# Kernel tuning notes

Measured on AMD Instinct MI355X. Metric: run time of the kernel, lower is better.

The kernel has to match this reference:

```python
import jax, jax.numpy as jnp
import numpy as np

EMB = 512       # emb_dim
H = 8           # n_heads
HD = EMB // H   # head_dim = 64
FREQ = 64       # freq_features
PERIOD = 0.1
N = 2048


def setup_inputs() -> dict:
    key = jax.random.key(0)
    ks = jax.random.split(key, 6)
    x = jax.random.normal(ks[0], (1, N, EMB), dtype=jnp.float32)
    v = jax.random.normal(ks[1], (1, N, 3), dtype=jnp.float32)
    vec_map = v / jnp.linalg.norm(v, axis=-1, keepdims=True)  # unit direction vectors
    s_in = 1.0 / np.sqrt(EMB)
    W_qkv = jax.random.normal(ks[2], (EMB, 3 * EMB), dtype=jnp.float32) * s_in
    b_qkv = jnp.zeros((3 * EMB,), dtype=jnp.float32)
    W_bias = jax.random.normal(ks[3], (FREQ, H), dtype=jnp.float32) * (1.0 / np.sqrt(FREQ))
    b_bias = jnp.zeros((H,), dtype=jnp.float32)
    W_out = jax.random.normal(ks[4], (EMB, EMB), dtype=jnp.float32) * s_in
    b_out = jnp.zeros((EMB,), dtype=jnp.float32)
    return {"x": x, "vec_map": vec_map, "W_qkv": W_qkv, "b_qkv": b_qkv,
            "W_bias": W_bias, "b_bias": b_bias, "W_out": W_out, "b_out": b_out}


def reference(x, vec_map, W_qkv, b_qkv, W_bias, b_bias, W_out, b_out):
    batch_dim = x.shape[:-2]
    n = x.shape[-2]
    # QKV projection -> (*, N, H, 3, HD)
    qkv = (x @ W_qkv + b_qkv).reshape(*batch_dim, n, H, 3, HD)
    q, k, v = (qkv[..., 0, :], qkv[..., 1, :], qkv[..., 2, :])
    # attention scores (*, Q, K, H), softmax over the K axis (axis=-2)
    attn = jnp.einsum('...qht,...kht->...qkh', q, k) / np.sqrt(HD)
    attn = jax.nn.softmax(attn, axis=-2)
    # relative bias from pairwise angles between direction vectors
    dot = jnp.einsum('...nc,...mc->...nm', vec_map, vec_map)
    angle = jnp.arccos(jnp.clip(dot, 0.0, 1.0)) / 0.001
    freqs = jnp.linspace(0.0, 1.0, FREQ // 2, dtype=jnp.float32) / PERIOD
    phase = freqs * angle[..., None]                      # (*, N, N, FREQ/2)
    pos = jnp.concatenate((jnp.sin(phase), jnp.cos(phase)), axis=-1)  # (*, N, N, FREQ)
    bias = pos @ W_bias + b_bias                          # (*, N, N, H)
    attn = attn + bias
    # weighted sum of values -> (*, N, EMB)
    y = jnp.einsum('...qkh,...kht->...qht', attn, v).reshape(*batch_dim, n, EMB)
    return y @ W_out + b_out
```

## Files before the change

kernel.cpp:

```cpp
#include <hip/hip_runtime.h>
#include <hip/hip_bf16.h>
#include <math.h>

#define NT 2048
#define EMBD 512
#define NH 8
#define QKV_LD 1536
#define KSPLIT 8

typedef unsigned short u16;
typedef __attribute__((ext_vector_type(8))) short short8;
typedef __attribute__((ext_vector_type(4))) float v4f;

static __device__ __forceinline__ float bf2f(unsigned int u) {
    union { unsigned int i; float f; } c; c.i = u << 16; return c.f;
}
static __device__ __forceinline__ unsigned int f2bf(float x) {
    union { float f; unsigned int u; } c; c.f = x;
    return (c.u + 0x7fffu + ((c.u >> 16) & 1u)) >> 16;
}
static __device__ __forceinline__ unsigned int cvtpk(float lo, float hi) {
    unsigned int r;
    asm("v_cvt_pk_bf16_f32 %0, %1, %2" : "=v"(r) : "v"(lo), "v"(hi));
    return r;
}

__global__ __launch_bounds__(256) void prep(const float* __restrict__ x,
    u16* __restrict__ xh, u16* __restrict__ xl,
    const float* __restrict__ Wqkv, u16* __restrict__ wth, u16* __restrict__ wtl,
    const float* __restrict__ Wout, u16* __restrict__ woth, u16* __restrict__ wotl)
{
    __shared__ float tile[64][65];
    int b = blockIdx.x;
    const int t = threadIdx.x;
    if (b < 1024) {
        int i = (b * 256 + t) << 2;
        float4 v = *(const float4*)(x + i);
        float f[4] = {v.x, v.y, v.z, v.w};
        unsigned int hi[4], lo[4];
#pragma unroll
        for (int j = 0; j < 4; ++j) {
            hi[j] = f2bf(f[j]);
            lo[j] = f2bf(f[j] - bf2f(hi[j]));
        }
        uint2 wh; wh.x = hi[0] | (hi[1] << 16); wh.y = hi[2] | (hi[3] << 16);
        uint2 wl; wl.x = lo[0] | (lo[1] << 16); wl.y = lo[2] | (lo[3] << 16);
        *(uint2*)(xh + i) = wh;
        *(uint2*)(xl + i) = wl;
        return;
    }
    b -= 1024;
    const float* W; u16* th; u16* tl; int ld, bx, by;
    if (b < 192) { W = Wqkv; th = wth;  tl = wtl;  ld = QKV_LD; bx = b % 24; by = b / 24; }
    else { b -= 192; W = Wout; th = woth; tl = wotl; ld = EMBD; bx = b & 7; by = b >> 3; }
    const int n0 = bx << 6, k0 = by << 6;
    const int r = t >> 2, c4 = (t & 3) << 4;
#pragma unroll
    for (int j = 0; j < 4; ++j)
        *(float4*)&tile[r][c4 + (j << 2)] =
            *(const float4*)(W + (size_t)(k0 + r) * ld + n0 + c4 + (j << 2));
    __syncthreads();
    const int n_l = t >> 2;
    u16 vh[16], vl[16];
#pragma unroll
    for (int j = 0; j < 16; ++j) {
        float f = tile[c4 + j][n_l];
        unsigned int h = f2bf(f);
        vh[j] = (u16)h;
        vl[j] = (u16)f2bf(f - bf2f(h));
    }
    u16* dh = th + (size_t)(n0 + n_l) * EMBD + k0 + c4;
    u16* dl = tl + (size_t)(n0 + n_l) * EMBD + k0 + c4;
    *(uint4*)dh       = *(uint4*)&vh[0];
    *(uint4*)(dh + 8) = *(uint4*)&vh[8];
    *(uint4*)dl       = *(uint4*)&vl[0];
    *(uint4*)(dl + 8) = *(uint4*)&vl[8];
}

__global__ __launch_bounds__(256) void gemm_qkv_mfma(const u16* __restrict__ xh,
    const u16* __restrict__ xl, const u16* __restrict__ wth,
    const u16* __restrict__ wtl, const float* __restrict__ bias,
    u16* __restrict__ qkvb)
{
    const int n0 = blockIdx.x << 6, m0 = blockIdx.y << 6;
    const int w = threadIdx.x >> 6, lane = threadIdx.x & 63;
    const int wm = w >> 1, wn = w & 1;
    const int fr = lane & 15, kd = (lane >> 4) << 3;

    const u16* ah0 = xh + (size_t)(m0 + wm * 32 + fr) * EMBD + kd;
    const u16* al0 = xl + (size_t)(m0 + wm * 32 + fr) * EMBD + kd;
    const u16* bh0 = wth + (size_t)(n0 + wn * 32 + fr) * EMBD + kd;
    const u16* bl0 = wtl + (size_t)(n0 + wn * 32 + fr) * EMBD + kd;

    v4f acc[2][2] = {};
    for (int kc = 0; kc < EMBD; kc += 32) {
        short8 a_h[2], a_l[2], b_h[2], b_l[2];
#pragma unroll
        for (int im = 0; im < 2; ++im) {
            a_h[im] = *(const short8*)(ah0 + (size_t)im * 16 * EMBD + kc);
            a_l[im] = *(const short8*)(al0 + (size_t)im * 16 * EMBD + kc);
        }
#pragma unroll
        for (int in = 0; in < 2; ++in) {
            b_h[in] = *(const short8*)(bh0 + (size_t)in * 16 * EMBD + kc);
            b_l[in] = *(const short8*)(bl0 + (size_t)in * 16 * EMBD + kc);
        }
#pragma unroll
        for (int im = 0; im < 2; ++im)
#pragma unroll
            for (int in = 0; in < 2; ++in) {
                acc[im][in] = __builtin_amdgcn_mfma_f32_16x16x32_bf16(a_h[im], b_h[in], acc[im][in], 0, 0, 0);
                acc[im][in] = __builtin_amdgcn_mfma_f32_16x16x32_bf16(a_h[im], b_l[in], acc[im][in], 0, 0, 0);
                acc[im][in] = __builtin_amdgcn_mfma_f32_16x16x32_bf16(a_l[im], b_h[in], acc[im][in], 0, 0, 0);
            }
    }
    const int qr = (lane >> 4) << 2;
#pragma unroll
    for (int im = 0; im < 2; ++im)
#pragma unroll
        for (int in = 0; in < 2; ++in) {
            int n = n0 + wn * 32 + in * 16 + fr;
            float bv = bias[n];
#pragma unroll
            for (int r = 0; r < 4; ++r) {
                int m = m0 + wm * 32 + im * 16 + qr + r;
                qkvb[(size_t)m * QKV_LD + n] = (u16)f2bf(acc[im][in][r] + bv);
            }
        }
}

__global__ __launch_bounds__(256) void transpose_v(const u16* __restrict__ qkvb,
                                                   u16* __restrict__ Vt)
{
    __shared__ u16 tile[64][72];
    const int h = blockIdx.y, k0 = blockIdx.x << 6;
    const int t = threadIdx.x;
    {
        int r = t >> 2, cg = (t & 3) << 4;
        const u16* src = qkvb + (size_t)(k0 + r) * QKV_LD + h * 192 + 128 + cg;
        *(uint4*)&tile[r][cg]     = *(const uint4*)src;
        *(uint4*)&tile[r][cg + 8] = *(const uint4*)(src + 8);
    }
    __syncthreads();
    {
        int c = t >> 2, kg = (t & 3) << 4;
        u16 tmp[16];
#pragma unroll
        for (int j = 0; j < 16; ++j) tmp[j] = tile[kg + j][c];
        u16* dst = Vt + ((size_t)h * 64 + c) * NT + k0 + kg;
        *(uint4*)dst       = *(uint4*)&tmp[0];
        *(uint4*)(dst + 8) = *(uint4*)&tmp[8];
    }
}

__global__ __launch_bounds__(512, 2) void attn_pv(
    const u16* __restrict__ qkvb, const u16* __restrict__ Vt,
    float* __restrict__ zpart, float* __restrict__ partsP)
{
    __shared__ u16 tile[8 * 2056];

    const int bid = blockIdx.x;
    const int zsp = bid & 7;
    const int qt  = bid >> 3;
    const int q0 = qt << 5;
    const int kbase = zsp << 8;

    const int t = threadIdx.x;
    const int w = t >> 6;
    const int lane = t & 63;
    const int fr = lane & 15;
    const int hi4 = lane >> 4;
    const int kd = hi4 << 3;
    const int qr = hi4 << 2;

    short8 aq[2][2];
#pragma unroll
    for (int mb = 0; mb < 2; ++mb)
#pragma unroll
        for (int kk = 0; kk < 2; ++kk)
            aq[mb][kk] = *(const short8*)(qkvb +
                (size_t)(q0 + mb * 16 + fr) * QKV_LD + w * 192 + kk * 32 + kd);

    v4f accP[2][4] = {};
    float zacc[2][4] = {};

    for (int c = 0; c < 4; ++c) {
        const int kc = kbase + (c << 6);
        short8 vb[4][2], bk[4][2];
#pragma unroll
        for (int nt = 0; nt < 4; ++nt)
#pragma unroll
            for (int kk = 0; kk < 2; ++kk) {
                vb[nt][kk] = *(const short8*)(Vt +
                    (size_t)(w * 64 + nt * 16 + fr) * NT + kc + kk * 32 + kd);
                bk[nt][kk] = *(const short8*)(qkvb +
                    (size_t)(kc + nt * 16 + fr) * QKV_LD + w * 192 + 64 + kk * 32 + kd);
            }
        v4f sacc[2][4] = {};
#pragma unroll
        for (int mb = 0; mb < 2; ++mb)
#pragma unroll
            for (int nt = 0; nt < 4; ++nt) {
                sacc[mb][nt] = __builtin_amdgcn_mfma_f32_16x16x32_bf16(aq[mb][0], bk[nt][0], sacc[mb][nt], 0, 0, 0);
                sacc[mb][nt] = __builtin_amdgcn_mfma_f32_16x16x32_bf16(aq[mb][1], bk[nt][1], sacc[mb][nt], 0, 0, 0);
            }
        unsigned int pk[2][4][2];
#pragma unroll
        for (int mb = 0; mb < 2; ++mb)
#pragma unroll
            for (int nt = 0; nt < 4; ++nt)
#pragma unroll
                for (int r2 = 0; r2 < 2; ++r2) {
                    float e0 = __expf(sacc[mb][nt][2 * r2] * 0.125f);
                    float e1 = __expf(sacc[mb][nt][2 * r2 + 1] * 0.125f);
                    zacc[mb][2 * r2] += e0;
                    zacc[mb][2 * r2 + 1] += e1;
                    pk[mb][nt][r2] = cvtpk(e0, e1);
                }
#pragma unroll
        for (int mb = 0; mb < 2; ++mb)
#pragma unroll
            for (int nt = 0; nt < 4; ++nt) {
                const int kg = (nt << 1) + (fr >> 3);
#pragma unroll
                for (int r = 0; r < 4; ++r) {
                    const int q = mb * 16 + qr + r;
                    tile[w * 2056 + q * 64 + ((kg ^ (q & 7)) << 3) + (fr & 7)] =
                        (u16)(pk[mb][nt][r >> 1] >> ((r & 1) << 4));
                }
            }
#pragma unroll
        for (int mb = 0; mb < 2; ++mb) {
            const int q = mb * 16 + fr;
#pragma unroll
            for (int kk = 0; kk < 2; ++kk) {
                short8 ap = *(const short8*)&tile[w * 2056 + q * 64 +
                    (((kk * 4 + hi4) ^ (q & 7)) << 3)];
#pragma unroll
                for (int nt = 0; nt < 4; ++nt)
                    accP[mb][nt] = __builtin_amdgcn_mfma_f32_16x16x32_bf16(ap, vb[nt][kk], accP[mb][nt], 0, 0, 0);
            }
        }
    }
#pragma unroll
    for (int off = 1; off < 16; off <<= 1)
#pragma unroll
        for (int mb = 0; mb < 2; ++mb)
#pragma unroll
            for (int r = 0; r < 4; ++r)
                zacc[mb][r] += __shfl_xor(zacc[mb][r], off);
    if (fr == 0) {
#pragma unroll
        for (int mb = 0; mb < 2; ++mb)
#pragma unroll
            for (int r = 0; r < 4; ++r)
                zpart[((size_t)zsp * 8 + w) * NT + q0 + mb * 16 + qr + r] = zacc[mb][r];
    }
    float* pP = partsP + (size_t)zsp * NT * EMBD;
#pragma unroll
    for (int mb = 0; mb < 2; ++mb)
#pragma unroll
        for (int nt = 0; nt < 4; ++nt)
#pragma unroll
            for (int r = 0; r < 4; ++r)
                pP[(size_t)(q0 + mb * 16 + qr + r) * EMBD +
                   (w << 6) + (nt << 4) + fr] = accP[mb][nt][r];
}

__global__ __launch_bounds__(512, 4) void bias_v(
    const u16* __restrict__ Vt, const float* __restrict__ vec,
    const float* __restrict__ Wb, const float* __restrict__ bb,
    float* __restrict__ partsB)
{
    __shared__ float flds[32];
    __shared__ float vql[96];
    __shared__ float ang[32 * 65];
    __shared__ u16 tile[8 * 2056];

    const int bid = blockIdx.x;
    const int zsp = bid & 7;
    const int qt  = bid >> 3;
    const int q0 = qt << 5;
    const int kbase = zsp << 8;

    const int t = threadIdx.x;
    const int w = t >> 6;
    const int lane = t & 63;
    const int fr = lane & 15;
    const int hi4 = lane >> 4;
    const int kd = hi4 << 3;
    const int qr = hi4 << 2;

    if (t < 32) flds[t] = __fdiv_rn(__fdiv_rn((float)t, 31.0f), 0.1f);
    else if (t < 128) vql[t - 32] = vec[q0 * 3 + (t - 32)];

    short8 BS, BC;
#pragma unroll
    for (int j = 0; j < 8; ++j) {
        float ws = (fr < 8) ? Wb[(kd + j) * 8 + fr] : 0.0f;
        float wc = (fr < 8) ? Wb[(32 + kd + j) * 8 + fr] : 0.0f;
        BS[j] = (short)f2bf(ws);
        BC[j] = (short)f2bf(wc);
    }
    const float bbv = (fr < 8) ? bb[fr] : 0.0f;

    v4f accB[2][4] = {};

    __syncthreads();

    for (int c = 0; c < 4; ++c) {
        const int kc = kbase + (c << 6);
        {
            const int p0 = t << 2;
            const int q = p0 >> 6;
            const int kl = p0 & 63;
            const float a0 = vql[q * 3], a1 = vql[q * 3 + 1], a2 = vql[q * 3 + 2];
            const float* vk = vec + (size_t)(kc + kl) * 3;
#pragma unroll
            for (int j = 0; j < 4; ++j) {
                float c0 = vk[j * 3], c1 = vk[j * 3 + 1], c2 = vk[j * 3 + 2];
                float dot = __fadd_rn(__fadd_rn(__fmul_rn(a0, c0), __fmul_rn(a1, c1)),
                                      __fmul_rn(a2, c2));
                float dotc = fminf(fmaxf(dot, 0.0f), 1.0f);
                ang[q * 65 + kl + j] = __fdiv_rn(acosf(dotc), 0.001f);
            }
        }
        __syncthreads();
#pragma unroll
        for (int gi = 0; gi < 16; ++gi) {
            const int g = w + (gi << 3);
            const int q = g >> 2;
            const int ksub = (g & 3) << 4;
            const float av = ang[q * 65 + ksub + fr];
            float sv[8], cv[8];
#pragma unroll
            for (int j = 0; j < 8; ++j) {
                float ph = __fmul_rn(flds[kd + j], av);
                float rv = ph * 0.15915494309189535f;
                float rf = rv - floorf(rv);
                sv[j] = __builtin_amdgcn_sinf(rf);
                cv[j] = __builtin_amdgcn_cosf(rf);
            }
            union { uint4 u; short8 v; } As, Ac;
            As.u.x = cvtpk(sv[0], sv[1]); As.u.y = cvtpk(sv[2], sv[3]);
            As.u.z = cvtpk(sv[4], sv[5]); As.u.w = cvtpk(sv[6], sv[7]);
            Ac.u.x = cvtpk(cv[0], cv[1]); Ac.u.y = cvtpk(cv[2], cv[3]);
            Ac.u.z = cvtpk(cv[4], cv[5]); Ac.u.w = cvtpk(cv[6], cv[7]);
            v4f cb = {};
            cb = __builtin_amdgcn_mfma_f32_16x16x32_bf16(As.v, BS, cb, 0, 0, 0);
            cb = __builtin_amdgcn_mfma_f32_16x16x32_bf16(Ac.v, BC, cb, 0, 0, 0);
            if (fr < 8) {
                const int kg = (ksub + qr) >> 3;
                uint2 wv;
                wv.x = cvtpk(cb[0] + bbv, cb[1] + bbv);
                wv.y = cvtpk(cb[2] + bbv, cb[3] + bbv);
                *(uint2*)&tile[fr * 2056 + q * 64 + ((kg ^ (q & 7)) << 3) + (qr & 7)] = wv;
            }
        }
        __syncthreads();
#pragma unroll
        for (int kk = 0; kk < 2; ++kk) {
            const int q0l = 0 * 16 + fr, q1l = 1 * 16 + fr;
            short8 ab0 = *(const short8*)&tile[w * 2056 + q0l * 64 +
                (((kk * 4 + hi4) ^ (q0l & 7)) << 3)];
            short8 ab1 = *(const short8*)&tile[w * 2056 + q1l * 64 +
                (((kk * 4 + hi4) ^ (q1l & 7)) << 3)];
#pragma unroll
            for (int nt = 0; nt < 4; ++nt) {
                short8 vbx = *(const short8*)(Vt +
                    (size_t)(w * 64 + nt * 16 + fr) * NT + kc + kk * 32 + kd);
                accB[0][nt] = __builtin_amdgcn_mfma_f32_16x16x32_bf16(ab0, vbx, accB[0][nt], 0, 0, 0);
                accB[1][nt] = __builtin_amdgcn_mfma_f32_16x16x32_bf16(ab1, vbx, accB[1][nt], 0, 0, 0);
            }
        }
    }
    float* pB = partsB + (size_t)zsp * NT * EMBD;
#pragma unroll
    for (int mb = 0; mb < 2; ++mb)
#pragma unroll
        for (int nt = 0; nt < 4; ++nt)
#pragma unroll
            for (int r = 0; r < 4; ++r)
                pB[(size_t)(q0 + mb * 16 + qr + r) * EMBD +
                   (w << 6) + (nt << 4) + fr] = accB[mb][nt][r];
}

__global__ __launch_bounds__(256) void reduce_y2(const float* __restrict__ partsP,
    const float* __restrict__ partsB, const float* __restrict__ zpart,
    u16* __restrict__ yh, u16* __restrict__ yl)
{
    const int MN = NT * EMBD;
    int i = (blockIdx.x * 256 + threadIdx.x) << 2;
    const int q = i >> 9;
    const int h = (i & 511) >> 6;
    float zs = 0.0f;
#pragma unroll
    for (int z = 0; z < KSPLIT; ++z) zs += zpart[((size_t)z * 8 + h) * NT + q];
    float4 aP = *(const float4*)(partsP + i);
    float4 aB = *(const float4*)(partsB + i);
#pragma unroll
    for (int z = 1; z < KSPLIT; ++z) {
        float4 p = *(const float4*)(partsP + (size_t)z * MN + i);
        float4 b = *(const float4*)(partsB + (size_t)z * MN + i);
        aP.x += p.x; aP.y += p.y; aP.z += p.z; aP.w += p.w;
        aB.x += b.x; aB.y += b.y; aB.z += b.z; aB.w += b.w;
    }
    const float iz = 1.0f / zs;
    float f[4] = {aP.x * iz + aB.x, aP.y * iz + aB.y,
                  aP.z * iz + aB.z, aP.w * iz + aB.w};
    unsigned int hi[4], lo[4];
#pragma unroll
    for (int j = 0; j < 4; ++j) {
        hi[j] = f2bf(f[j]);
        lo[j] = f2bf(f[j] - bf2f(hi[j]));
    }
    uint2 wh; wh.x = hi[0] | (hi[1] << 16); wh.y = hi[2] | (hi[3] << 16);
    uint2 wl; wl.x = lo[0] | (lo[1] << 16); wl.y = lo[2] | (lo[3] << 16);
    *(uint2*)(yh + i) = wh;
    *(uint2*)(yl + i) = wl;
}

__global__ __launch_bounds__(256) void gemm_out_mfma(const u16* __restrict__ yh,
    const u16* __restrict__ yl, const u16* __restrict__ wh,
    const u16* __restrict__ wl, const float* __restrict__ bias,
    float* __restrict__ out)
{
    const int n0 = blockIdx.x << 6, m0 = blockIdx.y << 6;
    const int w = threadIdx.x >> 6, lane = threadIdx.x & 63;
    const int wm = w >> 1, wn = w & 1;
    const int fr = lane & 15, kd = (lane >> 4) << 3;

    const u16* ah0 = yh + (size_t)(m0 + wm * 32 + fr) * EMBD + kd;
    const u16* al0 = yl + (size_t)(m0 + wm * 32 + fr) * EMBD + kd;
    const u16* bh0 = wh + (size_t)(n0 + wn * 32 + fr) * EMBD + kd;
    const u16* bl0 = wl + (size_t)(n0 + wn * 32 + fr) * EMBD + kd;

    v4f acc[2][2] = {};
    for (int kc = 0; kc < EMBD; kc += 32) {
        short8 a_h[2], a_l[2], b_h[2], b_l[2];
#pragma unroll
        for (int im = 0; im < 2; ++im) {
            a_h[im] = *(const short8*)(ah0 + (size_t)im * 16 * EMBD + kc);
            a_l[im] = *(const short8*)(al0 + (size_t)im * 16 * EMBD + kc);
        }
#pragma unroll
        for (int in = 0; in < 2; ++in) {
            b_h[in] = *(const short8*)(bh0 + (size_t)in * 16 * EMBD + kc);
            b_l[in] = *(const short8*)(bl0 + (size_t)in * 16 * EMBD + kc);
        }
#pragma unroll
        for (int im = 0; im < 2; ++im)
#pragma unroll
            for (int in = 0; in < 2; ++in) {
                acc[im][in] = __builtin_amdgcn_mfma_f32_16x16x32_bf16(a_h[im], b_h[in], acc[im][in], 0, 0, 0);
                acc[im][in] = __builtin_amdgcn_mfma_f32_16x16x32_bf16(a_h[im], b_l[in], acc[im][in], 0, 0, 0);
                acc[im][in] = __builtin_amdgcn_mfma_f32_16x16x32_bf16(a_l[im], b_h[in], acc[im][in], 0, 0, 0);
            }
    }
    const int qr = (lane >> 4) << 2;
#pragma unroll
    for (int im = 0; im < 2; ++im)
#pragma unroll
        for (int in = 0; in < 2; ++in) {
            int n = n0 + wn * 32 + in * 16 + fr;
            float bv = bias[n];
#pragma unroll
            for (int r = 0; r < 4; ++r) {
                int m = m0 + wm * 32 + im * 16 + qr + r;
                out[(size_t)m * EMBD + n] = acc[im][in][r] + bv;
            }
        }
}

extern "C" void kernel_launch(void* const* d_in, const int* in_sizes, int n_in,
                              void* d_out, int out_size, void* d_ws, size_t ws_size,
                              hipStream_t stream)
{
    const float* x    = (const float*)d_in[0];
    const float* vec  = (const float*)d_in[1];
    const float* Wqkv = (const float*)d_in[2];
    const float* bqkv = (const float*)d_in[3];
    const float* Wb   = (const float*)d_in[4];
    const float* bb   = (const float*)d_in[5];
    const float* Wout = (const float*)d_in[6];
    const float* bout = (const float*)d_in[7];
    float* out = (float*)d_out;

    char* ws = (char*)d_ws;
    u16*   qkvb   = (u16*)(ws);
    u16*   Vt     = (u16*)(ws + 6291456);
    float* zpart  = (float*)(ws + 8388608);
    float* partsP = (float*)(ws + 8912896);
    float* partsB = (float*)(ws + 42467328);
    u16*   yh     = (u16*)(ws + 76021760);
    u16*   yl     = (u16*)(ws + 78118912);
    u16*   xh     = (u16*)(ws + 80216064);
    u16*   xl     = (u16*)(ws + 82313216);
    u16*   wth    = (u16*)(ws + 84410368);
    u16*   wtl    = (u16*)(ws + 85983232);
    u16*   woth   = (u16*)(ws + 87556096);
    u16*   wotl   = (u16*)(ws + 88080384);

    prep<<<1280, 256, 0, stream>>>(x, xh, xl, Wqkv, wth, wtl, Wout, woth, wotl);
    gemm_qkv_mfma<<<dim3(24, 32), 256, 0, stream>>>(xh, xl, wth, wtl, bqkv, qkvb);
    transpose_v<<<dim3(32, 8), 256, 0, stream>>>(qkvb, Vt);
    bias_v<<<64 * KSPLIT, 512, 0, stream>>>(Vt, vec, Wb, bb, partsB);
    attn_pv<<<64 * KSPLIT, 512, 0, stream>>>(qkvb, Vt, zpart, partsP);
    reduce_y2<<<1024, 256, 0, stream>>>(partsP, partsB, zpart, yh, yl);
    gemm_out_mfma<<<dim3(8, 32), 256, 0, stream>>>(yh, yl, woth, wotl, bout, out);
}
```

Before: 245.2 us.

## Merge bias and attention kernels into one launch with block-parity dispatch

Combines the bias_v and attn_pv kernels into a single attn_bias kernel launched with twice as many blocks. Even-parity blocks run the angle/sin-cos bias path and odd-parity blocks run the QK-softmax-PV path. The aim is to drop one launch and let the transcendental-heavy bias blocks overlap with the MFMA/memory-heavy attention blocks on the same CUs. The cost is the larger combined shared-memory footprint and the shared launch bound (512,2), which may lower occupancy for the bias path compared with its former (512,4).

```diff
diff --git a/kernel.cpp b/kernel.cpp
--- a/kernel.cpp
+++ b/kernel.cpp
@@ -153,15 +153,21 @@
     }
 }
 
-__global__ __launch_bounds__(512, 2) void attn_pv(
+__global__ __launch_bounds__(512, 2) void attn_bias(
     const u16* __restrict__ qkvb, const u16* __restrict__ Vt,
-    float* __restrict__ zpart, float* __restrict__ partsP)
-{
+    const float* __restrict__ vec, const float* __restrict__ Wb,
+    const float* __restrict__ bb, float* __restrict__ zpart,
+    float* __restrict__ partsP, float* __restrict__ partsB)
+{
+    __shared__ float flds[32];
+    __shared__ float vql[96];
+    __shared__ float ang[32 * 65];
     __shared__ u16 tile[8 * 2056];
 
     const int bid = blockIdx.x;
     const int zsp = bid & 7;
-    const int qt  = bid >> 3;
+    const int par = (bid >> 3) & 1;
+    const int qt  = bid >> 4;
     const int q0 = qt << 5;
     const int kbase = zsp << 8;
 
@@ -173,216 +179,193 @@
     const int kd = hi4 << 3;
     const int qr = hi4 << 2;
 
-    short8 aq[2][2];
-#pragma unroll
-    for (int mb = 0; mb < 2; ++mb)
-#pragma unroll
-        for (int kk = 0; kk < 2; ++kk)
-            aq[mb][kk] = *(const short8*)(qkvb +
-                (size_t)(q0 + mb * 16 + fr) * QKV_LD + w * 192 + kk * 32 + kd);
-
-    v4f accP[2][4] = {};
-    float zacc[2][4] = {};
-
-    for (int c = 0; c < 4; ++c) {
-        const int kc = kbase + (c << 6);
-        short8 vb[4][2], bk[4][2];
-#pragma unroll
-        for (int nt = 0; nt < 4; ++nt)
+    if (par == 0) {
+        if (t < 32) flds[t] = __fdiv_rn(__fdiv_rn((float)t, 31.0f), 0.1f);
+        else if (t < 128) vql[t - 32] = vec[q0 * 3 + (t - 32)];
+
+        short8 BS, BC;
+#pragma unroll
+        for (int j = 0; j < 8; ++j) {
+            float ws = (fr < 8) ? Wb[(kd + j) * 8 + fr] : 0.0f;
+            float wc = (fr < 8) ? Wb[(32 + kd + j) * 8 + fr] : 0.0f;
+            BS[j] = (short)f2bf(ws);
+            BC[j] = (short)f2bf(wc);
+        }
+        const float bbv = (fr < 8) ? bb[fr] : 0.0f;
+
+        v4f accB[2][4] = {};
+
+        __syncthreads();
+
+        for (int c = 0; c < 4; ++c) {
+            const int kc = kbase + (c << 6);
+            {
+                const int p0 = t << 2;
+                const int q = p0 >> 6;
+                const int kl = p0 & 63;
+                const float a0 = vql[q * 3], a1 = vql[q * 3 + 1], a2 = vql[q * 3 + 2];
+                const float* vk = vec + (size_t)(kc + kl) * 3;
+#pragma unroll
+                for (int j = 0; j < 4; ++j) {
+                    float c0 = vk[j * 3], c1 = vk[j * 3 + 1], c2 = vk[j * 3 + 2];
+                    float dot = __fadd_rn(__fadd_rn(__fmul_rn(a0, c0), __fmul_rn(a1, c1)),
+                                          __fmul_rn(a2, c2));
+                    float dotc = fminf(fmaxf(dot, 0.0f), 1.0f);
+                    ang[q * 65 + kl + j] = __fdiv_rn(acosf(dotc), 0.001f);
+                }
+            }
+            __syncthreads();
+#pragma unroll
+            for (int gi = 0; gi < 16; ++gi) {
+                const int g = w + (gi << 3);
+                const int q = g >> 2;
+                const int ksub = (g & 3) << 4;
+                const float av = ang[q * 65 + ksub + fr];
+                float sv[8], cv[8];
+#pragma unroll
+                for (int j = 0; j < 8; ++j) {
+                    float ph = __fmul_rn(flds[kd + j], av);
+                    float rv = ph * 0.15915494309189535f;
+                    float rf = rv - floorf(rv);
+                    sv[j] = __builtin_amdgcn_sinf(rf);
+                    cv[j] = __builtin_amdgcn_cosf(rf);
+                }
+                union { uint4 u; short8 v; } As, Ac;
+                As.u.x = cvtpk(sv[0], sv[1]); As.u.y = cvtpk(sv[2], sv[3]);
+                As.u.z = cvtpk(sv[4], sv[5]); As.u.w = cvtpk(sv[6], sv[7]);
+                Ac.u.x = cvtpk(cv[0], cv[1]); Ac.u.y = cvtpk(cv[2], cv[3]);
+                Ac.u.z = cvtpk(cv[4], cv[5]); Ac.u.w = cvtpk(cv[6], cv[7]);
+                v4f cb = {};
+                cb = __builtin_amdgcn_mfma_f32_16x16x32_bf16(As.v, BS, cb, 0, 0, 0);
+                cb = __builtin_amdgcn_mfma_f32_16x16x32_bf16(Ac.v, BC, cb, 0, 0, 0);
+                if (fr < 8) {
+                    const int kg = (ksub + qr) >> 3;
+                    uint2 wv;
+                    wv.x = cvtpk(cb[0] + bbv, cb[1] + bbv);
+                    wv.y = cvtpk(cb[2] + bbv, cb[3] + bbv);
+                    *(uint2*)&tile[fr * 2056 + q * 64 + ((kg ^ (q & 7)) << 3) + (qr & 7)] = wv;
+                }
+            }
+            __syncthreads();
 #pragma unroll
             for (int kk = 0; kk < 2; ++kk) {
-                vb[nt][kk] = *(const short8*)(Vt +
-                    (size_t)(w * 64 + nt * 16 + fr) * NT + kc + kk * 32 + kd);
-                bk[nt][kk] = *(const short8*)(qkvb +
-                    (size_t)(kc + nt * 16 + fr) * QKV_LD + w * 192 + 64 + kk * 32 + kd);
-            }
-        v4f sacc[2][4] = {};
+                const int q0l = 0 * 16 + fr, q1l = 1 * 16 + fr;
+                short8 ab0 = *(const short8*)&tile[w * 2056 + q0l * 64 +
+                    (((kk * 4 + hi4) ^ (q0l & 7)) << 3)];
+                short8 ab1 = *(const short8*)&tile[w * 2056 + q1l * 64 +
+                    (((kk * 4 + hi4) ^ (q1l & 7)) << 3)];
+#pragma unroll
+                for (int nt = 0; nt < 4; ++nt) {
+                    short8 vbx = *(const short8*)(Vt +
+                        (size_t)(w * 64 + nt * 16 + fr) * NT + kc + kk * 32 + kd);
+                    accB[0][nt] = __builtin_amdgcn_mfma_f32_16x16x32_bf16(ab0, vbx, accB[0][nt], 0, 0, 0);
+                    accB[1][nt] = __builtin_amdgcn_mfma_f32_16x16x32_bf16(ab1, vbx, accB[1][nt], 0, 0, 0);
+                }
+            }
+        }
+        float* pB = partsB + (size_t)zsp * NT * EMBD;
 #pragma unroll
         for (int mb = 0; mb < 2; ++mb)
 #pragma unroll
-            for (int nt = 0; nt < 4; ++nt) {
-                sacc[mb][nt] = __builtin_amdgcn_mfma_f32_16x16x32_bf16(aq[mb][0], bk[nt][0], sacc[mb][nt], 0, 0, 0);
-                sacc[mb][nt] = __builtin_amdgcn_mfma_f32_16x16x32_bf16(aq[mb][1], bk[nt][1], sacc[mb][nt], 0, 0, 0);
-            }
-        unsigned int pk[2][4][2];
+            for (int nt = 0; nt < 4; ++nt)
+#pragma unroll
+                for (int r = 0; r < 4; ++r)
+                    pB[(size_t)(q0 + mb * 16 + qr + r) * EMBD +
+                       (w << 6) + (nt << 4) + fr] = accB[mb][nt][r];
+    } else {
+        short8 aq[2][2];
 #pragma unroll
         for (int mb = 0; mb < 2; ++mb)
 #pragma unroll
+            for (int kk = 0; kk < 2; ++kk)
+                aq[mb][kk] = *(const short8*)(qkvb +
+                    (size_t)(q0 + mb * 16 + fr) * QKV_LD + w * 192 + kk * 32 + kd);
+
+        v4f accP[2][4] = {};
+        float zacc[2][4] = {};
+
+        for (int c = 0; c < 4; ++c) {
+            const int kc = kbase + (c << 6);
+            short8 vb[4][2], bk[4][2];
+#pragma unroll
             for (int nt = 0; nt < 4; ++nt)
 #pragma unroll
-                for (int r2 = 0; r2 < 2; ++r2) {
-                    float e0 = __expf(sacc[mb][nt][2 * r2] * 0.125f);
-                    float e1 = __expf(sacc[mb][nt][2 * r2 + 1] * 0.125f);
-                    zacc[mb][2 * r2] += e0;
-                    zacc[mb][2 * r2 + 1] += e1;
-                    pk[mb][nt][r2] = cvtpk(e0, e1);
-                }
+                for (int kk = 0; kk < 2; ++kk) {
+                    vb[nt][kk] = *(const short8*)(Vt +
+                        (size_t)(w * 64 + nt * 16 + fr) * NT + kc + kk * 32 + kd);
+                    bk[nt][kk] = *(const short8*)(qkvb +
+                        (size_t)(kc + nt * 16 + fr) * QKV_LD + w * 192 + 64 + kk * 32 + kd);
+                }
+            v4f sacc[2][4] = {};
+#pragma unroll
+            for (int mb = 0; mb < 2; ++mb)
+#pragma unroll
+                for (int nt = 0; nt < 4; ++nt) {
+                    sacc[mb][nt] = __builtin_amdgcn_mfma_f32_16x16x32_bf16(aq[mb][0], bk[nt][0], sacc[mb][nt], 0, 0, 0);
+                    sacc[mb][nt] = __builtin_amdgcn_mfma_f32_16x16x32_bf16(aq[mb][1], bk[nt][1], sacc[mb][nt], 0, 0, 0);
+                }
+            unsigned int pk[2][4][2];
+#pragma unroll
+            for (int mb = 0; mb < 2; ++mb)
+#pragma unroll
+                for (int nt = 0; nt < 4; ++nt)
+#pragma unroll
+                    for (int r2 = 0; r2 < 2; ++r2) {
+                        float e0 = __expf(sacc[mb][nt][2 * r2] * 0.125f);
+                        float e1 = __expf(sacc[mb][nt][2 * r2 + 1] * 0.125f);
+                        zacc[mb][2 * r2] += e0;
+                        zacc[mb][2 * r2 + 1] += e1;
+                        pk[mb][nt][r2] = cvtpk(e0, e1);
+                    }
+#pragma unroll
+            for (int mb = 0; mb < 2; ++mb)
+#pragma unroll
+                for (int nt = 0; nt < 4; ++nt) {
+                    const int kg = (nt << 1) + (fr >> 3);
+#pragma unroll
+                    for (int r = 0; r < 4; ++r) {
+                        const int q = mb * 16 + qr + r;
+                        tile[w * 2056 + q * 64 + ((kg ^ (q & 7)) << 3) + (fr & 7)] =
+                            (u16)(pk[mb][nt][r >> 1] >> ((r & 1) << 4));
+                    }
+                }
+#pragma unroll
+            for (int mb = 0; mb < 2; ++mb) {
+                const int q = mb * 16 + fr;
+#pragma unroll
+                for (int kk = 0; kk < 2; ++kk) {
+                    short8 ap = *(const short8*)&tile[w * 2056 + q * 64 +
+                        (((kk * 4 + hi4) ^ (q & 7)) << 3)];
+#pragma unroll
+                    for (int nt = 0; nt < 4; ++nt)
+                        accP[mb][nt] = __builtin_amdgcn_mfma_f32_16x16x32_bf16(ap, vb[nt][kk], accP[mb][nt], 0, 0, 0);
+                }
+            }
+        }
+#pragma unroll
+        for (int off = 1; off < 16; off <<= 1)
+#pragma unroll
+            for (int mb = 0; mb < 2; ++mb)
+#pragma unroll
+                for (int r = 0; r < 4; ++r)
+                    zacc[mb][r] += __shfl_xor(zacc[mb][r], off);
+        if (fr == 0) {
+#pragma unroll
+            for (int mb = 0; mb < 2; ++mb)
+#pragma unroll
+                for (int r = 0; r < 4; ++r)
+                    zpart[((size_t)zsp * 8 + w) * NT + q0 + mb * 16 + qr + r] = zacc[mb][r];
+        }
+        float* pP = partsP + (size_t)zsp * NT * EMBD;
 #pragma unroll
         for (int mb = 0; mb < 2; ++mb)
 #pragma unroll
-            for (int nt = 0; nt < 4; ++nt) {
-                const int kg = (nt << 1) + (fr >> 3);
-#pragma unroll
-                for (int r = 0; r < 4; ++r) {
-                    const int q = mb * 16 + qr + r;
-                    tile[w * 2056 + q * 64 + ((kg ^ (q & 7)) << 3) + (fr & 7)] =
-                        (u16)(pk[mb][nt][r >> 1] >> ((r & 1) << 4));
-                }
-            }
-#pragma unroll
-        for (int mb = 0; mb < 2; ++mb) {
-            const int q = mb * 16 + fr;
-#pragma unroll
-            for (int kk = 0; kk < 2; ++kk) {
-                short8 ap = *(const short8*)&tile[w * 2056 + q * 64 +
-                    (((kk * 4 + hi4) ^ (q & 7)) << 3)];
-#pragma unroll
-                for (int nt = 0; nt < 4; ++nt)
-                    accP[mb][nt] = __builtin_amdgcn_mfma_f32_16x16x32_bf16(ap, vb[nt][kk], accP[mb][nt], 0, 0, 0);
-            }
-        }
-    }
-#pragma unroll
-    for (int off = 1; off < 16; off <<= 1)
-#pragma unroll
-        for (int mb = 0; mb < 2; ++mb)
-#pragma unroll
-            for (int r = 0; r < 4; ++r)
-                zacc[mb][r] += __shfl_xor(zacc[mb][r], off);
-    if (fr == 0) {
-#pragma unroll
-        for (int mb = 0; mb < 2; ++mb)
-#pragma unroll
-            for (int r = 0; r < 4; ++r)
-                zpart[((size_t)zsp * 8 + w) * NT + q0 + mb * 16 + qr + r] = zacc[mb][r];
-    }
-    float* pP = partsP + (size_t)zsp * NT * EMBD;
-#pragma unroll
-    for (int mb = 0; mb < 2; ++mb)
-#pragma unroll
-        for (int nt = 0; nt < 4; ++nt)
-#pragma unroll
-            for (int r = 0; r < 4; ++r)
-                pP[(size_t)(q0 + mb * 16 + qr + r) * EMBD +
-                   (w << 6) + (nt << 4) + fr] = accP[mb][nt][r];
-}
-
-__global__ __launch_bounds__(512, 4) void bias_v(
-    const u16* __restrict__ Vt, const float* __restrict__ vec,
-    const float* __restrict__ Wb, const float* __restrict__ bb,
-    float* __restrict__ partsB)
-{
-    __shared__ float flds[32];
-    __shared__ float vql[96];
-    __shared__ float ang[32 * 65];
-    __shared__ u16 tile[8 * 2056];
-
-    const int bid = blockIdx.x;
-    const int zsp = bid & 7;
-    const int qt  = bid >> 3;
-    const int q0 = qt << 5;
-    const int kbase = zsp << 8;
-
-    const int t = threadIdx.x;
-    const int w = t >> 6;
-    const int lane = t & 63;
-    const int fr = lane & 15;
-    const int hi4 = lane >> 4;
-    const int kd = hi4 << 3;
-    const int qr = hi4 << 2;
-
-    if (t < 32) flds[t] = __fdiv_rn(__fdiv_rn((float)t, 31.0f), 0.1f);
-    else if (t < 128) vql[t - 32] = vec[q0 * 3 + (t - 32)];
-
-    short8 BS, BC;
-#pragma unroll
-    for (int j = 0; j < 8; ++j) {
-        float ws = (fr < 8) ? Wb[(kd + j) * 8 + fr] : 0.0f;
-        float wc = (fr < 8) ? Wb[(32 + kd + j) * 8 + fr] : 0.0f;
-        BS[j] = (short)f2bf(ws);
-        BC[j] = (short)f2bf(wc);
-    }
-    const float bbv = (fr < 8) ? bb[fr] : 0.0f;
-
-    v4f accB[2][4] = {};
-
-    __syncthreads();
-
-    for (int c = 0; c < 4; ++c) {
-        const int kc = kbase + (c << 6);
-        {
-            const int p0 = t << 2;
-            const int q = p0 >> 6;
-            const int kl = p0 & 63;
-            const float a0 = vql[q * 3], a1 = vql[q * 3 + 1], a2 = vql[q * 3 + 2];
-            const float* vk = vec + (size_t)(kc + kl) * 3;
-#pragma unroll
-            for (int j = 0; j < 4; ++j) {
-                float c0 = vk[j * 3], c1 = vk[j * 3 + 1], c2 = vk[j * 3 + 2];
-                float dot = __fadd_rn(__fadd_rn(__fmul_rn(a0, c0), __fmul_rn(a1, c1)),
-                                      __fmul_rn(a2, c2));
-                float dotc = fminf(fmaxf(dot, 0.0f), 1.0f);
-                ang[q * 65 + kl + j] = __fdiv_rn(acosf(dotc), 0.001f);
-            }
-        }
-        __syncthreads();
-#pragma unroll
-        for (int gi = 0; gi < 16; ++gi) {
-            const int g = w + (gi << 3);
-            const int q = g >> 2;
-            const int ksub = (g & 3) << 4;
-            const float av = ang[q * 65 + ksub + fr];
-            float sv[8], cv[8];
-#pragma unroll
-            for (int j = 0; j < 8; ++j) {
-                float ph = __fmul_rn(flds[kd + j], av);
-                float rv = ph * 0.15915494309189535f;
-                float rf = rv - floorf(rv);
-                sv[j] = __builtin_amdgcn_sinf(rf);
-                cv[j] = __builtin_amdgcn_cosf(rf);
-            }
-            union { uint4 u; short8 v; } As, Ac;
-            As.u.x = cvtpk(sv[0], sv[1]); As.u.y = cvtpk(sv[2], sv[3]);
-            As.u.z = cvtpk(sv[4], sv[5]); As.u.w = cvtpk(sv[6], sv[7]);
-            Ac.u.x = cvtpk(cv[0], cv[1]); Ac.u.y = cvtpk(cv[2], cv[3]);
-            Ac.u.z = cvtpk(cv[4], cv[5]); Ac.u.w = cvtpk(cv[6], cv[7]);
-            v4f cb = {};
-            cb = __builtin_amdgcn_mfma_f32_16x16x32_bf16(As.v, BS, cb, 0, 0, 0);
-            cb = __builtin_amdgcn_mfma_f32_16x16x32_bf16(Ac.v, BC, cb, 0, 0, 0);
-            if (fr < 8) {
-                const int kg = (ksub + qr) >> 3;
-                uint2 wv;
-                wv.x = cvtpk(cb[0] + bbv, cb[1] + bbv);
-                wv.y = cvtpk(cb[2] + bbv, cb[3] + bbv);
-                *(uint2*)&tile[fr * 2056 + q * 64 + ((kg ^ (q & 7)) << 3) + (qr & 7)] = wv;
-            }
-        }
-        __syncthreads();
-#pragma unroll
-        for (int kk = 0; kk < 2; ++kk) {
-            const int q0l = 0 * 16 + fr, q1l = 1 * 16 + fr;
-            short8 ab0 = *(const short8*)&tile[w * 2056 + q0l * 64 +
-                (((kk * 4 + hi4) ^ (q0l & 7)) << 3)];
-            short8 ab1 = *(const short8*)&tile[w * 2056 + q1l * 64 +
-                (((kk * 4 + hi4) ^ (q1l & 7)) << 3)];
-#pragma unroll
-            for (int nt = 0; nt < 4; ++nt) {
-                short8 vbx = *(const short8*)(Vt +
-                    (size_t)(w * 64 + nt * 16 + fr) * NT + kc + kk * 32 + kd);
-                accB[0][nt] = __builtin_amdgcn_mfma_f32_16x16x32_bf16(ab0, vbx, accB[0][nt], 0, 0, 0);
-                accB[1][nt] = __builtin_amdgcn_mfma_f32_16x16x32_bf16(ab1, vbx, accB[1][nt], 0, 0, 0);
-            }
-        }
-    }
-    float* pB = partsB + (size_t)zsp * NT * EMBD;
-#pragma unroll
-    for (int mb = 0; mb < 2; ++mb)
-#pragma unroll
-        for (int nt = 0; nt < 4; ++nt)
-#pragma unroll
-            for (int r = 0; r < 4; ++r)
-                pB[(size_t)(q0 + mb * 16 + qr + r) * EMBD +
-                   (w << 6) + (nt << 4) + fr] = accB[mb][nt][r];
+            for (int nt = 0; nt < 4; ++nt)
+#pragma unroll
+                for (int r = 0; r < 4; ++r)
+                    pP[(size_t)(q0 + mb * 16 + qr + r) * EMBD +
+                       (w << 6) + (nt << 4) + fr] = accP[mb][nt][r];
+    }
 }
 
 __global__ __launch_bounds__(256) void reduce_y2(const float* __restrict__ partsP,
@@ -504,8 +487,8 @@
     prep<<<1280, 256, 0, stream>>>(x, xh, xl, Wqkv, wth, wtl, Wout, woth, wotl);
     gemm_qkv_mfma<<<dim3(24, 32), 256, 0, stream>>>(xh, xl, wth, wtl, bqkv, qkvb);
     transpose_v<<<dim3(32, 8), 256, 0, stream>>>(qkvb, Vt);
-    bias_v<<<64 * KSPLIT, 512, 0, stream>>>(Vt, vec, Wb, bb, partsB);
-    attn_pv<<<64 * KSPLIT, 512, 0, stream>>>(qkvb, Vt, zpart, partsP);
+    attn_bias<<<128 * KSPLIT, 512, 0, stream>>>(qkvb, Vt, vec, Wb, bb,
+                                                zpart, partsP, partsB);
     reduce_y2<<<1024, 256, 0, stream>>>(partsP, partsB, zpart, yh, yl);
     gemm_out_mfma<<<dim3(8, 32), 256, 0, stream>>>(yh, yl, woth, wotl, bout, out);
 }
```

Result: slower. 286.8 us (+16.9%).
